# Optimization experiments

Hardware: AMD Instinct MI355X
Metric: run time of the kernel (lower is better)

The kernel has to match this reference:

```python
import jax, jax.numpy as jnp
import numpy as np

L = 50          # prot_field_size
NUM_ANGLES = 120
C = 2           # repr feature channels


def setup_inputs() -> dict:
    key = jax.random.key(0)
    ks = jax.random.split(key, 6)
    return {
        "receptor": jax.random.normal(ks[0], (8, 1, L, L), jnp.float32),
        "ligand":   jax.random.normal(ks[1], (8, 1, L, L), jnp.float32),
        "conv_w":   jax.random.normal(ks[2], (C, 1, 3, 3), jnp.float32) * 0.3,
        "conv_b":   jax.random.normal(ks[3], (C,), jnp.float32) * 0.1,
        "scorer_w": jax.random.normal(ks[4], (C * C,), jnp.float32),
        "scorer_b": jax.random.normal(ks[5], (1,), jnp.float32) * 0.1,
    }


def _repr(x, w, b):
    # simple conv representation: [B,1,L,L] -> [B,C,L,L]
    y = jax.lax.conv_general_dilated(x, w, (1, 1), "SAME",
                                     dimension_numbers=("NCHW", "OIHW", "NCHW"))
    return y + b[None, :, None, None]


def _rotate_all(feat, angles):
    # torch affine_grid + grid_sample (bilinear, zeros padding, align_corners=True)
    # feat [B,C,H,W], angles [A] -> [A,B,C,H,W]
    B, Cc, H, W = feat.shape
    xs = jnp.linspace(-1.0, 1.0, W)
    ys = jnp.linspace(-1.0, 1.0, H)
    gy, gx = jnp.meshgrid(ys, xs, indexing="ij")          # [H,W] normalized coords
    c = jnp.cos(angles)[:, None, None]
    s = jnp.sin(angles)[:, None, None]
    xr = c * gx + s * gy        # theta row0 = [cos, sin, 0]
    yr = -s * gx + c * gy       # theta row1 = [-sin, cos, 0]
    ix = (xr + 1.0) * 0.5 * (W - 1)   # [A,H,W] pixel coords
    iy = (yr + 1.0) * 0.5 * (H - 1)
    x0 = jnp.floor(ix)
    y0 = jnp.floor(iy)
    out = jnp.zeros((B, Cc) + ix.shape, feat.dtype)       # [B,C,A,H,W]
    for dx, dy in ((0, 0), (1, 0), (0, 1), (1, 1)):
        xc = x0 + dx
        yc = y0 + dy
        wgt = (1.0 - jnp.abs(ix - xc)) * (1.0 - jnp.abs(iy - yc))
        valid = (xc >= 0) & (xc < W) & (yc >= 0) & (yc < H)
        xi = jnp.clip(xc, 0, W - 1).astype(jnp.int32)
        yi = jnp.clip(yc, 0, H - 1).astype(jnp.int32)
        vals = feat[:, :, yi, xi]                          # [B,C,A,H,W]
        out = out + vals * (wgt * valid)[None, None]
    return jnp.transpose(out, (2, 0, 1, 3, 4))             # [A,B,C,H,W]


def _protein_conv(rec, lig):
    # FFT cross-correlation of all channel pairs, padded to 2L, quadrant-swapped
    # rec [B,C,L,L], lig [A,B,C,L,L] -> [A,B,C*C,2L,2L]
    F1 = jnp.fft.rfft2(jnp.pad(rec, ((0, 0), (0, 0), (0, L), (0, L))))
    F2 = jnp.fft.rfft2(jnp.pad(lig, ((0, 0), (0, 0), (0, 0), (0, L), (0, L))))
    prod = F1[None, :, :, None] * jnp.conj(F2[:, :, None, :])   # [A,B,C,C,2L,L+1]
    cc = jnp.fft.irfft2(prod, s=(2 * L, 2 * L))
    cc = jnp.fft.fftshift(cc, axes=(-2, -1))
    A, B = cc.shape[0], cc.shape[1]
    return cc.reshape(A, B, C * C, 2 * L, 2 * L)


def reference(receptor, ligand, conv_w, conv_b, scorer_w, scorer_b):
    angles = jnp.arange(NUM_ANGLES, dtype=jnp.float32) * (np.pi / NUM_ANGLES)
    rec_feat = _repr(receptor, conv_w, conv_b)
    lig_feat = _repr(ligand, conv_w, conv_b)
    lig_rot = _rotate_all(lig_feat, angles)                # [A,B,C,L,L]
    cc = _protein_conv(rec_feat, lig_rot)                  # [A,B,C*C,2L,2L]
    scores = jnp.einsum("abfxy,f->abxy", cc, scorer_w) + scorer_b[0]
    A, B, S, _ = scores.shape                              # S = 2L
    # global top-1 over (angle, x, y) per batch == top_list[batch][0]
    flat = jnp.transpose(scores, (1, 0, 2, 3)).reshape(B, A * S * S)
    idx = jnp.argmax(flat, axis=1)
    a = idx // (S * S)
    r = idx % (S * S)
    x = r // S
    y = r % S
    best_angles = angles[a][:, None]                       # [B,1]
    trans = jnp.stack([x - L, y - L], axis=1).astype(jnp.float32)  # [B,2]
    return best_angles, trans
```

## Files before the change

### kernel.cpp

```cpp
#include <hip/hip_runtime.h>

#define L 50
#define NA 120
#define NB 8
#define NPIX 2500
#define NFREQ 51
#define NFULL 100
#define IST 52
#define ISPEC (NFULL * IST)
#define PST 51
#define RST 53
#define AST 51
#define ASTEP 0.026179938779914944f
#define PHI   0.06283185307179586f

#define OFF_REC  0
#define OFF_LIG  40000
#define OFF_F1   80000
#define OFF_P2   246400
#define OFF_PVAL 11766400
#define OFF_PIDX 11767360

#define CROT(wx, wy, sx, sy) { float nx_ = fmaf(wx, sx, -(wy) * (sy)); \
                               float ny_ = fmaf(wx, sy,  (wy) * (sx)); \
                               wx = nx_; wy = ny_; }
#define CMAC(q, wx, wy, ax, ay) { ax = fmaf(q.x, wx, fmaf(-q.y, wy, ax)); \
                                  ay = fmaf(q.x, wy, fmaf( q.y, wx, ay)); }

__global__ __launch_bounds__(256) void k_conv(
    const float* __restrict__ rec, const float* __restrict__ lig,
    const float* __restrict__ cw, const float* __restrict__ cb,
    const float* __restrict__ sw,
    float* __restrict__ rec_feat, float* __restrict__ lig_comb) {
  int t = blockIdx.x * blockDim.x + threadIdx.x;
  if (t >= NB * NPIX) return;
  int b = t / NPIX, p = t % NPIX;
  int i = p / L, j = p % L;
  float r0 = cb[0], r1 = cb[1], l0 = cb[0], l1 = cb[1];
  for (int di = 0; di < 3; ++di) {
    int ii = i + di - 1;
    if (ii < 0 || ii >= L) continue;
    for (int dj = 0; dj < 3; ++dj) {
      int jj = j + dj - 1;
      if (jj < 0 || jj >= L) continue;
      float w0 = cw[di * 3 + dj], w1 = cw[9 + di * 3 + dj];
      float xv = rec[b * NPIX + ii * L + jj];
      float yv = lig[b * NPIX + ii * L + jj];
      r0 += w0 * xv; r1 += w1 * xv;
      l0 += w0 * yv; l1 += w1 * yv;
    }
  }
  rec_feat[(b * 2 + 0) * NPIX + p] = r0;
  rec_feat[(b * 2 + 1) * NPIX + p] = r1;
  lig_comb[(b * 2 + 0) * NPIX + p] = sw[0] * l0 + sw[1] * l1;
  lig_comb[(b * 2 + 1) * NPIX + p] = sw[2] * l0 + sw[3] * l1;
}

__device__ __forceinline__ void rowdft(const float* img, float2* Arow, int tid,
                                       int stride) {
  if (tid < 255) {
    const int kR = tid % 51, rgR = tid / 51;
    float are[10], aim[10];
#pragma unroll
    for (int t = 0; t < 10; ++t) { are[t] = 0.f; aim[t] = 0.f; }
    float stx, sty;
    sincosf(PHI * (float)kR, &sty, &stx); sty = -sty;
    for (int half = 0; half < 2; ++half) {
      int u0 = half ? 6 : 0, u1 = half ? 13 : 6;
      float wx, wy;
      int t0 = half ? (24 * kR) % 100 : 0;
      sincosf(PHI * (float)t0, &wy, &wx); wy = -wy;
      for (int u = u0; u < u1; ++u) {
        float4 q[10];
#pragma unroll
        for (int t = 0; t < 10; ++t)
          q[t] = *(const float4*)(img + (rgR + 5 * t) * 52 + 4 * u);
#pragma unroll
        for (int v = 0; v < 4; ++v) {
#pragma unroll
          for (int t = 0; t < 10; ++t) {
            float val = (v == 0) ? q[t].x : (v == 1) ? q[t].y : (v == 2) ? q[t].z : q[t].w;
            are[t] = fmaf(val, wx, are[t]);
            aim[t] = fmaf(val, wy, aim[t]);
          }
          CROT(wx, wy, stx, sty);
        }
      }
    }
#pragma unroll
    for (int t = 0; t < 10; ++t)
      Arow[(rgR + 5 * t) * stride + kR] = make_float2(are[t], aim[t]);
  }
}

__global__ __launch_bounds__(256, 3) void k_fwd_rec(
    const float* __restrict__ src, float2* __restrict__ F1w) {
  __shared__ __align__(16) float img[50 * 52];
  __shared__ __align__(16) float2 Arow[50 * RST + 8];
  const int tid = threadIdx.x;
  const int im = blockIdx.x % 16, kcB = blockIdx.x / 16;
  const int k0 = (kcB == 0) ? 0 : 11 + 10 * (kcB - 1);
  for (int o = tid; o < 50 * 52; o += 256) {
    int i = o / 52, j = o - i * 52;
    img[o] = (j < 50) ? src[im * NPIX + i * 50 + j] : 0.f;
  }
  __syncthreads();
  rowdft(img, Arow, tid, RST);
  __syncthreads();
  if (tid < 250) {
    const int mp = tid % 50, sub = tid / 50;
    int c0, cw;
    if (kcB == 0) { cw = (sub == 0) ? 3 : 2; c0 = (sub == 0) ? 0 : 1 + 2 * sub; }
    else          { cw = 2; c0 = 2 * sub; }
    float Ex[3], Ey[3], Ox[3], Oy[3];
#pragma unroll
    for (int i = 0; i < 3; ++i) { Ex[i] = 0.f; Ey[i] = 0.f; Ox[i] = 0.f; Oy[i] = 0.f; }
    float s2x, s2y;
    sincosf(PHI * (float)((2 * mp) % 100), &s2y, &s2x); s2y = -s2y;
    { float wx = 1.f, wy = 0.f;
      for (int s = 0; s < 25; ++s) {
        const float2* ap = Arow + (2 * s) * RST + k0 + c0;
#pragma unroll
        for (int i = 0; i < 3; ++i) { float2 q = ap[i]; CMAC(q, wx, wy, Ex[i], Ey[i]); }
        CROT(wx, wy, s2x, s2y);
      } }
    { float wx, wy;
      sincosf(PHI * (float)mp, &wy, &wx); wy = -wy;
      for (int s = 0; s < 25; ++s) {
        const float2* ap = Arow + (2 * s + 1) * RST + k0 + c0;
#pragma unroll
        for (int i = 0; i < 3; ++i) { float2 q = ap[i]; CMAC(q, wx, wy, Ox[i], Oy[i]); }
        CROT(wx, wy, s2x, s2y);
      } }
    float2* d0 = F1w + (size_t)im * ISPEC + mp * IST + k0 + c0;
    float2* d1 = d0 + 50 * IST;
#pragma unroll
    for (int i = 0; i < 3; ++i)
      if (i < cw) {
        d0[i] = make_float2(Ex[i] + Ox[i], Ey[i] + Oy[i]);
        d1[i] = make_float2(Ex[i] - Ox[i], Ey[i] - Oy[i]);
      }
  }
}

__global__ __launch_bounds__(256, 3) void k_fwd_prod(
    const float* __restrict__ lig_comb, const float2* __restrict__ F1,
    float2* __restrict__ P2) {
  __shared__ __align__(16) float img[50 * 52];
  __shared__ __align__(16) float2 Arow[2][52 * AST];
  const int tid = threadIdx.x;
  const int ab = blockIdx.x, a = ab / NB, b = ab % NB;
  float sa, ca; sincosf((float)a * ASTEP, &sa, &ca);

  for (int o = tid; o < 2 * 2 * AST; o += 256) {
    int f = o / (2 * AST), rem = o % (2 * AST);
    Arow[f][50 * AST + rem] = make_float2(0.f, 0.f);
  }

  for (int f = 0; f < 2; ++f) {
    const float* src = lig_comb + (b * 2 + f) * NPIX;
    for (int o = tid; o < 50 * 52; o += 256) {
      int i = o / 52, j = o - i * 52;
      float acc = 0.f;
      if (j < 50) {
        float gx = fmaf((float)j, 2.0f / 49.0f, -1.0f);
        float gy = fmaf((float)i, 2.0f / 49.0f, -1.0f);
        float ix = (ca * gx + sa * gy + 1.0f) * 24.5f;
        float iy = (ca * gy - sa * gx + 1.0f) * 24.5f;
        float x0 = floorf(ix), y0 = floorf(iy);
#pragma unroll
        for (int dy = 0; dy < 2; ++dy)
#pragma unroll
          for (int dx = 0; dx < 2; ++dx) {
            float xc = x0 + dx, yc = y0 + dy;
            float w = (1.0f - fabsf(ix - xc)) * (1.0f - fabsf(iy - yc));
            bool valid = (xc >= 0.f) && (xc < 50.f) && (yc >= 0.f) && (yc < 50.f);
            int xi = (int)fminf(fmaxf(xc, 0.f), 49.f);
            int yi = (int)fminf(fmaxf(yc, 0.f), 49.f);
            acc += valid ? w * src[yi * L + xi] : 0.f;
          }
      }
      img[o] = acc;
    }
    __syncthreads();
    rowdft(img, Arow[f], tid, AST);
    __syncthreads();
  }

  for (int pass = 0; pass < 2; ++pass) {
    const int v = pass * 256 + tid;
    if (v < 425) {
      const int mp = v % 25, c = v / 25;
      const int k0 = 3 * c;
      float Q0x[6], Q0y[6], Q1x[6], Q1y[6], Q2x[6], Q2y[6], Q3x[6], Q3y[6];
#pragma unroll
      for (int q = 0; q < 6; ++q) {
        Q0x[q] = 0.f; Q0y[q] = 0.f; Q1x[q] = 0.f; Q1y[q] = 0.f;
        Q2x[q] = 0.f; Q2y[q] = 0.f; Q3x[q] = 0.f; Q3y[q] = 0.f;
      }
      float s4x, s4y;
      sincosf(PHI * (float)((4 * mp) % 100), &s4y, &s4x); s4y = -s4y;
      float wx = 1.f, wy = 0.f;
      for (int s = 0; s < 13; ++s) {
        const float2* b0 = &Arow[0][(4 * s) * AST + k0];
        const float2* b1 = &Arow[1][(4 * s) * AST + k0];
#pragma unroll
        for (int i = 0; i < 3; ++i) {
          float2 q;
          q = b0[i];           CMAC(q, wx, wy, Q0x[i],     Q0y[i]);
          q = b0[AST + i];     CMAC(q, wx, wy, Q1x[i],     Q1y[i]);
          q = b0[2*AST + i];   CMAC(q, wx, wy, Q2x[i],     Q2y[i]);
          q = b0[3*AST + i];   CMAC(q, wx, wy, Q3x[i],     Q3y[i]);
          q = b1[i];           CMAC(q, wx, wy, Q0x[3 + i], Q0y[3 + i]);
          q = b1[AST + i];     CMAC(q, wx, wy, Q1x[3 + i], Q1y[3 + i]);
          q = b1[2*AST + i];   CMAC(q, wx, wy, Q2x[3 + i], Q2y[3 + i]);
          q = b1[3*AST + i];   CMAC(q, wx, wy, Q3x[3 + i], Q3y[3 + i]);
        }
        CROT(wx, wy, s4x, s4y);
      }
      float c1x, c1y; sincosf(PHI * (float)mp, &c1y, &c1x); c1y = -c1y;
      float c2x = fmaf(c1x, c1x, -c1y * c1y), c2y = 2.f * c1x * c1y;
      float c3x = fmaf(c2x, c1x, -c2y * c1y), c3y = fmaf(c2x, c1y, c2y * c1x);
      float4* dst = (float4*)(P2 + (size_t)ab * 5100 + v * 12);
#pragma unroll
      for (int i = 0; i < 3; ++i) {
        float px[4], py[4];
#pragma unroll
        for (int t = 0; t < 4; ++t) { px[t] = 0.f; py[t] = 0.f; }
#pragma unroll
        for (int ch = 0; ch < 2; ++ch) {
          const int q = ch * 3 + i;
          float u0x = Q0x[q], u0y = Q0y[q];
          float u1x = fmaf(c1x, Q1x[q], -c1y * Q1y[q]);
          float u1y = fmaf(c1x, Q1y[q],  c1y * Q1x[q]);
          float u2x = fmaf(c2x, Q2x[q], -c2y * Q2y[q]);
          float u2y = fmaf(c2x, Q2y[q],  c2y * Q2x[q]);
          float u3x = fmaf(c3x, Q3x[q], -c3y * Q3y[q]);
          float u3y = fmaf(c3x, Q3y[q],  c3y * Q3x[q]);
          float Axx = u0x + u2x, Ayy = u0y + u2y;
          float Bxx = u0x - u2x, Byy = u0y - u2y;
          float Cxx = u1x + u3x, Cyy = u1y + u3y;
          float Dxx = u1x - u3x, Dyy = u1y - u3y;
          float Gx[4], Gy[4];
          Gx[0] = Axx + Cxx; Gy[0] = Ayy + Cyy;
          Gx[2] = Axx - Cxx; Gy[2] = Ayy - Cyy;
          Gx[1] = Bxx + Dyy; Gy[1] = Byy - Dxx;
          Gx[3] = Bxx - Dyy; Gy[3] = Byy + Dxx;
          const float2* Fb = F1 + (size_t)(b * 2 + ch) * ISPEC + mp * IST + k0 + i;
#pragma unroll
          for (int t = 0; t < 4; ++t) {
            float2 Fv = Fb[t * 25 * IST];
            px[t] = fmaf(Fv.x, Gx[t], fmaf( Fv.y, Gy[t], px[t]));
            py[t] = fmaf(Fv.y, Gx[t], fmaf(-Fv.x, Gy[t], py[t]));
          }
        }
        dst[i * 2 + 0] = make_float4(px[0], py[0], px[1], py[1]);
        dst[i * 2 + 1] = make_float4(px[2], py[2], px[3], py[3]);
      }
    }
  }
}

__global__ __launch_bounds__(256, 4) void k_inv_argmax(
    const float2* __restrict__ P2, float* __restrict__ pval,
    int* __restrict__ pidx) {
  __shared__ __align__(16) float2 Pl[100 * PST];
  __shared__ float wr[4];
  __shared__ int wi[4];
  const int tid = threadIdx.x, ab = blockIdx.x;

  for (int h = 0; h < 2; ++h) {
    const int v = h * 256 + tid;
    if (v < 425) {
      const int mp = v % 25, c = v / 25, kk = 3 * c;
      const float4* s4 = (const float4*)(P2 + (size_t)ab * 5100 + v * 12);
#pragma unroll
      for (int i = 0; i < 3; ++i) {
        float4 q01 = s4[i * 2], q23 = s4[i * 2 + 1];
        Pl[(mp     ) * PST + kk + i] = make_float2(q01.x, q01.y);
        Pl[(mp + 25) * PST + kk + i] = make_float2(q01.z, q01.w);
        Pl[(mp + 50) * PST + kk + i] = make_float2(q23.x, q23.y);
        Pl[(mp + 75) * PST + kk + i] = make_float2(q23.z, q23.w);
      }
    }
  }
  __syncthreads();

  const int rp = tid % 25, kc = tid / 25;
  const int k0 = (kc < 3) ? 7 * kc : 21 + 6 * (kc - 3);
  const int CW = (kc < 3) ? 7 : 6;
  float Q0x[7], Q0y[7], Q1x[7], Q1y[7], Q2x[7], Q2y[7], Q3x[7], Q3y[7];
  if (tid < 200) {
#pragma unroll
    for (int q = 0; q < 7; ++q) {
      Q0x[q] = 0.f; Q0y[q] = 0.f; Q1x[q] = 0.f; Q1y[q] = 0.f;
      Q2x[q] = 0.f; Q2y[q] = 0.f; Q3x[q] = 0.f; Q3y[q] = 0.f;
    }
    float s4x, s4y;
    sincosf(PHI * (float)((4 * rp) % 100), &s4y, &s4x);
    float wx = 1.f, wy = 0.f;
    for (int s = 0; s < 25; ++s) {
      const float2* p0 = Pl + (4 * s) * PST + k0;
#pragma unroll
      for (int i = 0; i < 7; ++i) {
        float2 q;
        q = p0[i];           CMAC(q, wx, wy, Q0x[i], Q0y[i]);
        q = p0[PST + i];     CMAC(q, wx, wy, Q1x[i], Q1y[i]);
        q = p0[2*PST + i];   CMAC(q, wx, wy, Q2x[i], Q2y[i]);
        q = p0[3*PST + i];   CMAC(q, wx, wy, Q3x[i], Q3y[i]);
      }
      CROT(wx, wy, s4x, s4y);
    }
  }
  __syncthreads();
  if (tid < 200) {
    float c1x, c1y; sincosf(PHI * (float)rp, &c1y, &c1x);
    float c2x = fmaf(c1x, c1x, -c1y * c1y), c2y = 2.f * c1x * c1y;
    float c3x = fmaf(c2x, c1x, -c2y * c1y), c3y = fmaf(c2x, c1y, c2y * c1x);
#pragma unroll
    for (int i = 0; i < 7; ++i) {
      float u1x = fmaf(c1x, Q1x[i], -c1y * Q1y[i]);
      float u1y = fmaf(c1x, Q1y[i],  c1y * Q1x[i]);
      float u2x = fmaf(c2x, Q2x[i], -c2y * Q2y[i]);
      float u2y = fmaf(c2x, Q2y[i],  c2y * Q2x[i]);
      float u3x = fmaf(c3x, Q3x[i], -c3y * Q3y[i]);
      float u3y = fmaf(c3x, Q3y[i],  c3y * Q3x[i]);
      float Axx = Q0x[i] + u2x, Ayy = Q0y[i] + u2y;
      float Bxx = Q0x[i] - u2x, Byy = Q0y[i] - u2y;
      float Cxx = u1x + u3x,    Cyy = u1y + u3y;
      float Dxx = u1x - u3x,    Dyy = u1y - u3y;
      if (i < CW) {
        float2* Tk = Pl + (k0 + i) * NFULL;
        Tk[rp]      = make_float2(Axx + Cxx, Ayy + Cyy);
        Tk[rp + 25] = make_float2(Bxx - Dyy, Byy + Dxx);
        Tk[rp + 50] = make_float2(Axx - Cxx, Ayy - Cyy);
        Tk[rp + 75] = make_float2(Bxx + Dyy, Byy - Dxx);
      }
    }
  }
  __syncthreads();

  float best = -3.4e38f;
  int bidx = 0x7fffffff;
  if (tid < 200) {
    const int cp = tid % 50, rc = tid / 50;
    const int r0 = (rc < 2) ? rc * 26 : 52 + (rc - 2) * 24;
    const int RW = (rc < 2) ? 26 : 24;
    float e[26], o[26];
#pragma unroll
    for (int i = 0; i < 26; ++i) { e[i] = 0.f; o[i] = 0.f; }
    float stx, sty;
    sincosf(PHI * (float)((2 * cp) % 100), &sty, &stx);
    { float wx = stx, wy = sty;
      for (int s = 1; s < 25; ++s) {
        const float4* tp4 = (const float4*)(Pl + (2 * s) * NFULL + r0);
#pragma unroll
        for (int ii = 0; ii < 13; ++ii) {
          float4 q = tp4[ii];
          e[2*ii]   = fmaf(q.x, wx, fmaf(-q.y, wy, e[2*ii]));
          e[2*ii+1] = fmaf(q.z, wx, fmaf(-q.w, wy, e[2*ii+1]));
        }
        CROT(wx, wy, stx, sty);
      } }
    { float wx, wy;
      sincosf(PHI * (float)cp, &wy, &wx);
      for (int s = 0; s < 25; ++s) {
        const float4* tp4 = (const float4*)(Pl + (2 * s + 1) * NFULL + r0);
#pragma unroll
        for (int ii = 0; ii < 13; ++ii) {
          float4 q = tp4[ii];
          o[2*ii]   = fmaf(q.x, wx, fmaf(-q.y, wy, o[2*ii]));
          o[2*ii+1] = fmaf(q.z, wx, fmaf(-q.w, wy, o[2*ii+1]));
        }
        CROT(wx, wy, stx, sty);
      } }
    float sgn = (cp & 1) ? -1.f : 1.f;
    const float2* T0  = Pl + r0;
    const float2* T50 = Pl + 50 * NFULL + r0;
    const int ys0 = cp + 50, ys1 = cp;
#pragma unroll
    for (int i = 0; i < 26; ++i)
      if (i < RW) {
        int r = r0 + i;
        float base = T0[i].x + sgn * T50[i].x;
        float X0 = fmaf(2.f, e[i] + o[i], base);
        float X1 = fmaf(2.f, e[i] - o[i], base);
        int xs = r + 50; if (xs >= 100) xs -= 100;
        int f0 = xs * 100 + ys0, f1 = xs * 100 + ys1;
        if (X0 > best || (X0 == best && f0 < bidx)) { best = X0; bidx = f0; }
        if (X1 > best || (X1 == best && f1 < bidx)) { best = X1; bidx = f1; }
      }
  }
  for (int off = 32; off > 0; off >>= 1) {
    float ov = __shfl_down(best, off);
    int oi = __shfl_down(bidx, off);
    if (ov > best || (ov == best && oi < bidx)) { best = ov; bidx = oi; }
  }
  if ((tid & 63) == 0) { wr[tid >> 6] = best; wi[tid >> 6] = bidx; }
  __syncthreads();
  if (tid == 0) {
#pragma unroll
    for (int w = 1; w < 4; ++w) {
      if (wr[w] > best || (wr[w] == best && wi[w] < bidx)) { best = wr[w]; bidx = wi[w]; }
    }
    pval[ab] = best; pidx[ab] = (ab / NB) * 10000 + bidx;
  }
}

__global__ void k_final(const float* __restrict__ pval,
                        const int* __restrict__ pidx, float* __restrict__ out) {
  int b = threadIdx.x;
  if (b >= NB) return;
  float best = -3.4e38f; int bidx = 0x7fffffff;
  for (int a = 0; a < NA; ++a) {
    float v = pval[a * NB + b]; int ix = pidx[a * NB + b];
    if (v > best || (v == best && ix < bidx)) { best = v; bidx = ix; }
  }
  int a = bidx / 10000, rr = bidx % 10000, x = rr / NFULL, y = rr % NFULL;
  out[b] = a * ASTEP;
  out[NB + b * 2 + 0] = (float)(x - L);
  out[NB + b * 2 + 1] = (float)(y - L);
}

extern "C" void kernel_launch(void* const* d_in, const int* in_sizes, int n_in,
                              void* d_out, int out_size, void* d_ws, size_t ws_size,
                              hipStream_t stream) {
  const float* receptor = (const float*)d_in[0];
  const float* ligand   = (const float*)d_in[1];
  const float* conv_w   = (const float*)d_in[2];
  const float* conv_b   = (const float*)d_in[3];
  const float* scorer_w = (const float*)d_in[4];
  float* ws = (float*)d_ws;
  float* rec_feat = ws + OFF_REC;
  float* lig_comb = ws + OFF_LIG;
  float2* F1      = (float2*)(ws + OFF_F1);
  float2* P2      = (float2*)(ws + OFF_P2);
  float* pval     = ws + OFF_PVAL;
  int*   pidx     = (int*)(ws + OFF_PIDX);
  float* out      = (float*)d_out;

  k_conv<<<(NB * NPIX + 255) / 256, 256, 0, stream>>>(
      receptor, ligand, conv_w, conv_b, scorer_w, rec_feat, lig_comb);
  k_fwd_rec<<<80, 256, 0, stream>>>(rec_feat, F1);
  k_fwd_prod<<<NA * NB, 256, 0, stream>>>(lig_comb, F1, P2);
  k_inv_argmax<<<NA * NB, 256, 0, stream>>>(P2, pval, pidx);
  k_final<<<1, 64, 0, stream>>>(pval, pidx, out);
}
```

Baseline: 244.2 us.

## Fuse conv into receptor DFT kernel and repack inverse-DFT shared buffer

Removes the standalone conv kernel. Receptor features are now computed on the fly inside k_fwd_rec, and 8 extra blocks compute the ligand combined features. This saves one launch and a global round-trip. Separately, the inverse/argmax kernel's shared buffer drops from stride 51 to stride 50 with the 51st column stored apart, so float4 loads and 8-column chunks work over 175 threads. The risks are possible bank conflicts from the unpadded stride and redundant conv recomputation across the 5 kcB blocks per image.

```diff
diff --git a/kernel.cpp b/kernel.cpp
--- a/kernel.cpp
+++ b/kernel.cpp
@@ -8,13 +8,11 @@
 #define NFULL 100
 #define IST 52
 #define ISPEC (NFULL * IST)
-#define PST 51
 #define RST 53
 #define AST 51
 #define ASTEP 0.026179938779914944f
 #define PHI   0.06283185307179586f
 
-#define OFF_REC  0
 #define OFF_LIG  40000
 #define OFF_F1   80000
 #define OFF_P2   246400
@@ -26,35 +24,6 @@
                                wx = nx_; wy = ny_; }
 #define CMAC(q, wx, wy, ax, ay) { ax = fmaf(q.x, wx, fmaf(-q.y, wy, ax)); \
                                   ay = fmaf(q.x, wy, fmaf( q.y, wx, ay)); }
-
-__global__ __launch_bounds__(256) void k_conv(
-    const float* __restrict__ rec, const float* __restrict__ lig,
-    const float* __restrict__ cw, const float* __restrict__ cb,
-    const float* __restrict__ sw,
-    float* __restrict__ rec_feat, float* __restrict__ lig_comb) {
-  int t = blockIdx.x * blockDim.x + threadIdx.x;
-  if (t >= NB * NPIX) return;
-  int b = t / NPIX, p = t % NPIX;
-  int i = p / L, j = p % L;
-  float r0 = cb[0], r1 = cb[1], l0 = cb[0], l1 = cb[1];
-  for (int di = 0; di < 3; ++di) {
-    int ii = i + di - 1;
-    if (ii < 0 || ii >= L) continue;
-    for (int dj = 0; dj < 3; ++dj) {
-      int jj = j + dj - 1;
-      if (jj < 0 || jj >= L) continue;
-      float w0 = cw[di * 3 + dj], w1 = cw[9 + di * 3 + dj];
-      float xv = rec[b * NPIX + ii * L + jj];
-      float yv = lig[b * NPIX + ii * L + jj];
-      r0 += w0 * xv; r1 += w1 * xv;
-      l0 += w0 * yv; l1 += w1 * yv;
-    }
-  }
-  rec_feat[(b * 2 + 0) * NPIX + p] = r0;
-  rec_feat[(b * 2 + 1) * NPIX + p] = r1;
-  lig_comb[(b * 2 + 0) * NPIX + p] = sw[0] * l0 + sw[1] * l1;
-  lig_comb[(b * 2 + 1) * NPIX + p] = sw[2] * l0 + sw[3] * l1;
-}
 
 __device__ __forceinline__ void rowdft(const float* img, float2* Arow, int tid,
                                        int stride) {
@@ -94,24 +63,63 @@
 }
 
 __global__ __launch_bounds__(256, 3) void k_fwd_rec(
-    const float* __restrict__ src, float2* __restrict__ F1w) {
+    const float* __restrict__ rec, const float* __restrict__ lig,
+    const float* __restrict__ cw, const float* __restrict__ cb,
+    const float* __restrict__ sw,
+    float* __restrict__ lig_comb, float2* __restrict__ F1w) {
   __shared__ __align__(16) float img[50 * 52];
   __shared__ __align__(16) float2 Arow[50 * RST + 8];
   const int tid = threadIdx.x;
+  if (blockIdx.x >= 80) {
+    const int bb = blockIdx.x - 80;
+    for (int p = tid; p < NPIX; p += 256) {
+      int i = p / 50, j = p % 50;
+      float l0 = cb[0], l1 = cb[1];
+      for (int di = 0; di < 3; ++di) {
+        int ii = i + di - 1;
+        if (ii < 0 || ii >= 50) continue;
+        for (int dj = 0; dj < 3; ++dj) {
+          int jj = j + dj - 1;
+          if (jj < 0 || jj >= 50) continue;
+          float v = lig[bb * NPIX + ii * 50 + jj];
+          l0 += cw[di * 3 + dj] * v;
+          l1 += cw[9 + di * 3 + dj] * v;
+        }
+      }
+      lig_comb[(bb * 2 + 0) * NPIX + p] = sw[0] * l0 + sw[1] * l1;
+      lig_comb[(bb * 2 + 1) * NPIX + p] = sw[2] * l0 + sw[3] * l1;
+    }
+    return;
+  }
   const int im = blockIdx.x % 16, kcB = blockIdx.x / 16;
+  const int bb = im >> 1, cc = im & 1;
   const int k0 = (kcB == 0) ? 0 : 11 + 10 * (kcB - 1);
+  const float* rsrc = rec + bb * NPIX;
   for (int o = tid; o < 50 * 52; o += 256) {
     int i = o / 52, j = o - i * 52;
-    img[o] = (j < 50) ? src[im * NPIX + i * 50 + j] : 0.f;
+    float acc = 0.f;
+    if (j < 50) {
+      acc = cb[cc];
+      for (int di = 0; di < 3; ++di) {
+        int ii = i + di - 1;
+        if (ii < 0 || ii >= 50) continue;
+        for (int dj = 0; dj < 3; ++dj) {
+          int jj = j + dj - 1;
+          if (jj < 0 || jj >= 50) continue;
+          acc += cw[cc * 9 + di * 3 + dj] * rsrc[ii * 50 + jj];
+        }
+      }
+    }
+    img[o] = acc;
   }
   __syncthreads();
   rowdft(img, Arow, tid, RST);
   __syncthreads();
   if (tid < 250) {
     const int mp = tid % 50, sub = tid / 50;
-    int c0, cw;
-    if (kcB == 0) { cw = (sub == 0) ? 3 : 2; c0 = (sub == 0) ? 0 : 1 + 2 * sub; }
-    else          { cw = 2; c0 = 2 * sub; }
+    int c0, cwd;
+    if (kcB == 0) { cwd = (sub == 0) ? 3 : 2; c0 = (sub == 0) ? 0 : 1 + 2 * sub; }
+    else          { cwd = 2; c0 = 2 * sub; }
     float Ex[3], Ey[3], Ox[3], Oy[3];
 #pragma unroll
     for (int i = 0; i < 3; ++i) { Ex[i] = 0.f; Ey[i] = 0.f; Ox[i] = 0.f; Oy[i] = 0.f; }
@@ -136,7 +144,7 @@
     float2* d1 = d0 + 50 * IST;
 #pragma unroll
     for (int i = 0; i < 3; ++i)
-      if (i < cw) {
+      if (i < cwd) {
         d0[i] = make_float2(Ex[i] + Ox[i], Ey[i] + Oy[i]);
         d1[i] = make_float2(Ex[i] - Ox[i], Ey[i] - Oy[i]);
       }
@@ -264,7 +272,7 @@
 __global__ __launch_bounds__(256, 4) void k_inv_argmax(
     const float2* __restrict__ P2, float* __restrict__ pval,
     int* __restrict__ pidx) {
-  __shared__ __align__(16) float2 Pl[100 * PST];
+  __shared__ __align__(16) float2 buf[5100];
   __shared__ float wr[4];
   __shared__ int wi[4];
   const int tid = threadIdx.x, ab = blockIdx.x;
@@ -277,48 +285,80 @@
 #pragma unroll
       for (int i = 0; i < 3; ++i) {
         float4 q01 = s4[i * 2], q23 = s4[i * 2 + 1];
-        Pl[(mp     ) * PST + kk + i] = make_float2(q01.x, q01.y);
-        Pl[(mp + 25) * PST + kk + i] = make_float2(q01.z, q01.w);
-        Pl[(mp + 50) * PST + kk + i] = make_float2(q23.x, q23.y);
-        Pl[(mp + 75) * PST + kk + i] = make_float2(q23.z, q23.w);
+        int col = kk + i;
+        if (col < 50) {
+          buf[(mp     ) * 50 + col] = make_float2(q01.x, q01.y);
+          buf[(mp + 25) * 50 + col] = make_float2(q01.z, q01.w);
+          buf[(mp + 50) * 50 + col] = make_float2(q23.x, q23.y);
+          buf[(mp + 75) * 50 + col] = make_float2(q23.z, q23.w);
+        } else {
+          buf[5000 + mp     ] = make_float2(q01.x, q01.y);
+          buf[5000 + mp + 25] = make_float2(q01.z, q01.w);
+          buf[5000 + mp + 50] = make_float2(q23.x, q23.y);
+          buf[5000 + mp + 75] = make_float2(q23.z, q23.w);
+        }
       }
     }
   }
   __syncthreads();
 
   const int rp = tid % 25, kc = tid / 25;
-  const int k0 = (kc < 3) ? 7 * kc : 21 + 6 * (kc - 3);
-  const int CW = (kc < 3) ? 7 : 6;
-  float Q0x[7], Q0y[7], Q1x[7], Q1y[7], Q2x[7], Q2y[7], Q3x[7], Q3y[7];
-  if (tid < 200) {
-#pragma unroll
-    for (int q = 0; q < 7; ++q) {
+  const int k0 = 8 * kc;
+  float Q0x[8], Q0y[8], Q1x[8], Q1y[8], Q2x[8], Q2y[8], Q3x[8], Q3y[8];
+  if (tid < 175) {
+#pragma unroll
+    for (int q = 0; q < 8; ++q) {
       Q0x[q] = 0.f; Q0y[q] = 0.f; Q1x[q] = 0.f; Q1y[q] = 0.f;
       Q2x[q] = 0.f; Q2y[q] = 0.f; Q3x[q] = 0.f; Q3y[q] = 0.f;
     }
     float s4x, s4y;
     sincosf(PHI * (float)((4 * rp) % 100), &s4y, &s4x);
     float wx = 1.f, wy = 0.f;
-    for (int s = 0; s < 25; ++s) {
-      const float2* p0 = Pl + (4 * s) * PST + k0;
-#pragma unroll
-      for (int i = 0; i < 7; ++i) {
-        float2 q;
-        q = p0[i];           CMAC(q, wx, wy, Q0x[i], Q0y[i]);
-        q = p0[PST + i];     CMAC(q, wx, wy, Q1x[i], Q1y[i]);
-        q = p0[2*PST + i];   CMAC(q, wx, wy, Q2x[i], Q2y[i]);
-        q = p0[3*PST + i];   CMAC(q, wx, wy, Q3x[i], Q3y[i]);
-      }
-      CROT(wx, wy, s4x, s4y);
-    }
-  }
-  __syncthreads();
-  if (tid < 200) {
+    if (kc < 6) {
+      for (int s = 0; s < 25; ++s) {
+        const int rb = (4 * s) * 50 + k0;
+#pragma unroll
+        for (int j = 0; j < 4; ++j) {
+          const float4* p4 = (const float4*)(buf + rb + j * 50);
+          float* Qx = (j == 0) ? Q0x : (j == 1) ? Q1x : (j == 2) ? Q2x : Q3x;
+          float* Qy = (j == 0) ? Q0y : (j == 1) ? Q1y : (j == 2) ? Q2y : Q3y;
+#pragma unroll
+          for (int h = 0; h < 4; ++h) {
+            float4 q4 = p4[h];
+            float2 qa = make_float2(q4.x, q4.y), qb = make_float2(q4.z, q4.w);
+            CMAC(qa, wx, wy, Qx[2 * h],     Qy[2 * h]);
+            CMAC(qb, wx, wy, Qx[2 * h + 1], Qy[2 * h + 1]);
+          }
+        }
+        CROT(wx, wy, s4x, s4y);
+      }
+    } else {
+      for (int s = 0; s < 25; ++s) {
+        const int rb = (4 * s) * 50 + 48;
+        const int nb = 5000 + 4 * s;
+#pragma unroll
+        for (int j = 0; j < 4; ++j) {
+          float4 q4 = *(const float4*)(buf + rb + j * 50);
+          float2 q50 = buf[nb + j];
+          float2 qa = make_float2(q4.x, q4.y), qb = make_float2(q4.z, q4.w);
+          float* Qx = (j == 0) ? Q0x : (j == 1) ? Q1x : (j == 2) ? Q2x : Q3x;
+          float* Qy = (j == 0) ? Q0y : (j == 1) ? Q1y : (j == 2) ? Q2y : Q3y;
+          CMAC(qa,  wx, wy, Qx[0], Qy[0]);
+          CMAC(qb,  wx, wy, Qx[1], Qy[1]);
+          CMAC(q50, wx, wy, Qx[2], Qy[2]);
+        }
+        CROT(wx, wy, s4x, s4y);
+      }
+    }
+  }
+  __syncthreads();
+  if (tid < 175) {
+    const int CW = (kc < 6) ? 8 : 3;
     float c1x, c1y; sincosf(PHI * (float)rp, &c1y, &c1x);
     float c2x = fmaf(c1x, c1x, -c1y * c1y), c2y = 2.f * c1x * c1y;
     float c3x = fmaf(c2x, c1x, -c2y * c1y), c3y = fmaf(c2x, c1y, c2y * c1x);
 #pragma unroll
-    for (int i = 0; i < 7; ++i) {
+    for (int i = 0; i < 8; ++i) {
       float u1x = fmaf(c1x, Q1x[i], -c1y * Q1y[i]);
       float u1y = fmaf(c1x, Q1y[i],  c1y * Q1x[i]);
       float u2x = fmaf(c2x, Q2x[i], -c2y * Q2y[i]);
@@ -330,7 +370,7 @@
       float Cxx = u1x + u3x,    Cyy = u1y + u3y;
       float Dxx = u1x - u3x,    Dyy = u1y - u3y;
       if (i < CW) {
-        float2* Tk = Pl + (k0 + i) * NFULL;
+        float2* Tk = buf + (k0 + i) * NFULL;
         Tk[rp]      = make_float2(Axx + Cxx, Ayy + Cyy);
         Tk[rp + 25] = make_float2(Bxx - Dyy, Byy + Dxx);
         Tk[rp + 50] = make_float2(Axx - Cxx, Ayy - Cyy);
@@ -353,7 +393,7 @@
     sincosf(PHI * (float)((2 * cp) % 100), &sty, &stx);
     { float wx = stx, wy = sty;
       for (int s = 1; s < 25; ++s) {
-        const float4* tp4 = (const float4*)(Pl + (2 * s) * NFULL + r0);
+        const float4* tp4 = (const float4*)(buf + (2 * s) * NFULL + r0);
 #pragma unroll
         for (int ii = 0; ii < 13; ++ii) {
           float4 q = tp4[ii];
@@ -365,7 +405,7 @@
     { float wx, wy;
       sincosf(PHI * (float)cp, &wy, &wx);
       for (int s = 0; s < 25; ++s) {
-        const float4* tp4 = (const float4*)(Pl + (2 * s + 1) * NFULL + r0);
+        const float4* tp4 = (const float4*)(buf + (2 * s + 1) * NFULL + r0);
 #pragma unroll
         for (int ii = 0; ii < 13; ++ii) {
           float4 q = tp4[ii];
@@ -375,8 +415,8 @@
         CROT(wx, wy, stx, sty);
       } }
     float sgn = (cp & 1) ? -1.f : 1.f;
-    const float2* T0  = Pl + r0;
-    const float2* T50 = Pl + 50 * NFULL + r0;
+    const float2* T0  = buf + r0;
+    const float2* T50 = buf + 50 * NFULL + r0;
     const int ys0 = cp + 50, ys1 = cp;
 #pragma unroll
     for (int i = 0; i < 26; ++i)
@@ -431,7 +471,6 @@
   const float* conv_b   = (const float*)d_in[3];
   const float* scorer_w = (const float*)d_in[4];
   float* ws = (float*)d_ws;
-  float* rec_feat = ws + OFF_REC;
   float* lig_comb = ws + OFF_LIG;
   float2* F1      = (float2*)(ws + OFF_F1);
   float2* P2      = (float2*)(ws + OFF_P2);
@@ -439,9 +478,8 @@
   int*   pidx     = (int*)(ws + OFF_PIDX);
   float* out      = (float*)d_out;
 
-  k_conv<<<(NB * NPIX + 255) / 256, 256, 0, stream>>>(
-      receptor, ligand, conv_w, conv_b, scorer_w, rec_feat, lig_comb);
-  k_fwd_rec<<<80, 256, 0, stream>>>(rec_feat, F1);
+  k_fwd_rec<<<88, 256, 0, stream>>>(receptor, ligand, conv_w, conv_b, scorer_w,
+                                    lig_comb, F1);
   k_fwd_prod<<<NA * NB, 256, 0, stream>>>(lig_comb, F1, P2);
   k_inv_argmax<<<NA * NB, 256, 0, stream>>>(P2, pval, pidx);
   k_final<<<1, 64, 0, stream>>>(pval, pidx, out);
```

Result: slower. 255.3 us (+4.5%).

## Add extra radix-2 split to final inverse DFT stage, producing four outputs per column

Applied to the files above, without the earlier changes.

The last inverse-DFT pass is restructured so each thread handles 25 column phases instead of 50. Even and odd frequency rows are further split by index mod 4, so one set of twiddle accumulations yields four output columns (cp, cp+25, cp+50, cp+75) instead of two. This roughly halves the twiddle-multiply work per output and changes the row split across 8 groups of 12-14 rows. In exchange the odd branch must keep both real and imaginary accumulators, which raises register pressure and per-thread FMA count.

```diff
diff --git a/kernel.cpp b/kernel.cpp
--- a/kernel.cpp
+++ b/kernel.cpp
@@ -343,52 +343,96 @@
   float best = -3.4e38f;
   int bidx = 0x7fffffff;
   if (tid < 200) {
-    const int cp = tid % 50, rc = tid / 50;
-    const int r0 = (rc < 2) ? rc * 26 : 52 + (rc - 2) * 24;
-    const int RW = (rc < 2) ? 26 : 24;
-    float e[26], o[26];
-#pragma unroll
-    for (int i = 0; i < 26; ++i) { e[i] = 0.f; o[i] = 0.f; }
+    const int cp = tid % 25, rc8 = tid / 25;
+    const int r0 = (rc8 < 6) ? 12 * rc8 : 72 + 14 * (rc8 - 6);
+    const int RW = (rc8 < 6) ? 12 : 14;
+    float SP[14], SM[14], OPre[14], OPim[14], OMre[14], OMim[14];
+#pragma unroll
+    for (int i = 0; i < 14; ++i) {
+      SP[i] = 0.f; SM[i] = 0.f; OPre[i] = 0.f;
+      OPim[i] = 0.f; OMre[i] = 0.f; OMim[i] = 0.f;
+    }
     float stx, sty;
     sincosf(PHI * (float)((2 * cp) % 100), &sty, &stx);
     { float wx = stx, wy = sty;
-      for (int s = 1; s < 25; ++s) {
-        const float4* tp4 = (const float4*)(Pl + (2 * s) * NFULL + r0);
-#pragma unroll
-        for (int ii = 0; ii < 13; ++ii) {
-          float4 q = tp4[ii];
-          e[2*ii]   = fmaf(q.x, wx, fmaf(-q.y, wy, e[2*ii]));
-          e[2*ii+1] = fmaf(q.z, wx, fmaf(-q.w, wy, e[2*ii+1]));
+      for (int s2 = 0; s2 < 12; ++s2) {
+        const float4* tpA = (const float4*)(Pl + (4 * s2 + 2) * NFULL + r0);
+#pragma unroll
+        for (int h = 0; h < 7; ++h) {
+          float4 q = tpA[h];
+          SM[2*h]   = fmaf(q.x, wx, fmaf(-q.y, wy, SM[2*h]));
+          SM[2*h+1] = fmaf(q.z, wx, fmaf(-q.w, wy, SM[2*h+1]));
+        }
+        CROT(wx, wy, stx, sty);
+        const float4* tpB = (const float4*)(Pl + (4 * s2 + 4) * NFULL + r0);
+#pragma unroll
+        for (int h = 0; h < 7; ++h) {
+          float4 q = tpB[h];
+          SP[2*h]   = fmaf(q.x, wx, fmaf(-q.y, wy, SP[2*h]));
+          SP[2*h+1] = fmaf(q.z, wx, fmaf(-q.w, wy, SP[2*h+1]));
         }
         CROT(wx, wy, stx, sty);
       } }
     { float wx, wy;
       sincosf(PHI * (float)cp, &wy, &wx);
-      for (int s = 0; s < 25; ++s) {
-        const float4* tp4 = (const float4*)(Pl + (2 * s + 1) * NFULL + r0);
-#pragma unroll
-        for (int ii = 0; ii < 13; ++ii) {
-          float4 q = tp4[ii];
-          o[2*ii]   = fmaf(q.x, wx, fmaf(-q.y, wy, o[2*ii]));
-          o[2*ii+1] = fmaf(q.z, wx, fmaf(-q.w, wy, o[2*ii+1]));
+      for (int s2 = 0; s2 < 12; ++s2) {
+        const float4* tpA = (const float4*)(Pl + (4 * s2 + 1) * NFULL + r0);
+#pragma unroll
+        for (int h = 0; h < 7; ++h) {
+          float4 q = tpA[h];
+          OPre[2*h]   = fmaf(q.x, wx, fmaf(-q.y, wy, OPre[2*h]));
+          OPim[2*h]   = fmaf(q.x, wy, fmaf( q.y, wx, OPim[2*h]));
+          OPre[2*h+1] = fmaf(q.z, wx, fmaf(-q.w, wy, OPre[2*h+1]));
+          OPim[2*h+1] = fmaf(q.z, wy, fmaf( q.w, wx, OPim[2*h+1]));
         }
         CROT(wx, wy, stx, sty);
+        const float4* tpB = (const float4*)(Pl + (4 * s2 + 3) * NFULL + r0);
+#pragma unroll
+        for (int h = 0; h < 7; ++h) {
+          float4 q = tpB[h];
+          OMre[2*h]   = fmaf(q.x, wx, fmaf(-q.y, wy, OMre[2*h]));
+          OMim[2*h]   = fmaf(q.x, wy, fmaf( q.y, wx, OMim[2*h]));
+          OMre[2*h+1] = fmaf(q.z, wx, fmaf(-q.w, wy, OMre[2*h+1]));
+          OMim[2*h+1] = fmaf(q.z, wy, fmaf( q.w, wx, OMim[2*h+1]));
+        }
+        CROT(wx, wy, stx, sty);
+      }
+      { const float4* tp = (const float4*)(Pl + 49 * NFULL + r0);
+#pragma unroll
+        for (int h = 0; h < 7; ++h) {
+          float4 q = tp[h];
+          OPre[2*h]   = fmaf(q.x, wx, fmaf(-q.y, wy, OPre[2*h]));
+          OPim[2*h]   = fmaf(q.x, wy, fmaf( q.y, wx, OPim[2*h]));
+          OPre[2*h+1] = fmaf(q.z, wx, fmaf(-q.w, wy, OPre[2*h+1]));
+          OPim[2*h+1] = fmaf(q.z, wy, fmaf( q.w, wx, OPim[2*h+1]));
+        }
       } }
-    float sgn = (cp & 1) ? -1.f : 1.f;
+    float sgn0 = (cp & 1) ? -1.f : 1.f;
     const float2* T0  = Pl + r0;
     const float2* T50 = Pl + 50 * NFULL + r0;
-    const int ys0 = cp + 50, ys1 = cp;
-#pragma unroll
-    for (int i = 0; i < 26; ++i)
+#pragma unroll
+    for (int i = 0; i < 14; ++i)
       if (i < RW) {
         int r = r0 + i;
-        float base = T0[i].x + sgn * T50[i].x;
-        float X0 = fmaf(2.f, e[i] + o[i], base);
-        float X1 = fmaf(2.f, e[i] - o[i], base);
+        float t0x = T0[i].x, t50x = sgn0 * T50[i].x;
+        float b0 = t0x + t50x;
+        float b1 = t0x - t50x;
+        float e0 = SP[i] + SM[i],   e1 = SP[i] - SM[i];
+        float o0 = OPre[i] + OMre[i];
+        float o1 = OMim[i] - OPim[i];
+        float X0 = fmaf(2.f, e0 + o0, b0);
+        float X1 = fmaf(2.f, e0 - o0, b0);
+        float X2 = fmaf(2.f, e1 + o1, b1);
+        float X3 = fmaf(2.f, e1 - o1, b1);
         int xs = r + 50; if (xs >= 100) xs -= 100;
-        int f0 = xs * 100 + ys0, f1 = xs * 100 + ys1;
-        if (X0 > best || (X0 == best && f0 < bidx)) { best = X0; bidx = f0; }
-        if (X1 > best || (X1 == best && f1 < bidx)) { best = X1; bidx = f1; }
+        int g0 = xs * 100 + cp + 50;
+        int g1 = xs * 100 + cp;
+        int g2 = xs * 100 + cp + 75;
+        int g3 = xs * 100 + cp + 25;
+        if (X0 > best || (X0 == best && g0 < bidx)) { best = X0; bidx = g0; }
+        if (X1 > best || (X1 == best && g1 < bidx)) { best = X1; bidx = g1; }
+        if (X2 > best || (X2 == best && g2 < bidx)) { best = X2; bidx = g2; }
+        if (X3 > best || (X3 == best && g3 < bidx)) { best = X3; bidx = g3; }
       }
   }
   for (int off = 32; off > 0; off >>= 1) {
```

Measured after the change: 589.6 us. 2.41x slower.
